# Kernel tuning notes

Hardware: AMD Instinct MI355X
Metric: run time of the kernel (lower is better)

Reference implementation:

```python
import jax, jax.numpy as jnp
import numpy as np

B, T, D_IN, H, OUT = 256, 512, 128, 256, 128


def setup_inputs() -> dict:
    key = jax.random.key(0)
    ks = jax.random.split(key, 10)
    s_in = 1.0 / np.sqrt(H)
    inp = {
        "x": jax.random.normal(ks[0], (B, T, D_IN), dtype=jnp.float32),
        # layer 0 (PyTorch LSTM gate order: i, f, g, o along 4H)
        "W_ih0": jax.random.uniform(ks[1], (4 * H, D_IN), minval=-s_in, maxval=s_in),
        "W_hh0": jax.random.uniform(ks[2], (4 * H, H), minval=-s_in, maxval=s_in),
        "b_ih0": jax.random.uniform(ks[3], (4 * H,), minval=-s_in, maxval=s_in),
        "b_hh0": jax.random.uniform(ks[4], (4 * H,), minval=-s_in, maxval=s_in),
        # layer 1
        "W_ih1": jax.random.uniform(ks[5], (4 * H, H), minval=-s_in, maxval=s_in),
        "W_hh1": jax.random.uniform(ks[6], (4 * H, H), minval=-s_in, maxval=s_in),
        "b_ih1": jax.random.uniform(ks[7], (4 * H,), minval=-s_in, maxval=s_in),
        "b_hh1": jax.random.uniform(ks[8], (4 * H,), minval=-s_in, maxval=s_in),
        # fc head (bias=False)
        "W_fc": jax.random.uniform(ks[9], (OUT, H), minval=-s_in, maxval=s_in),
    }
    return inp


def _lstm_layer(x_seq, W_ih, W_hh, b_ih, b_hh):
    # x_seq: [B, T, D]; precompute input projection once (big GEMM),
    # leave only the small h@W_hh GEMM inside the sequential scan.
    b, t = x_seq.shape[0], x_seq.shape[1]
    h_dim = W_hh.shape[1]
    x_proj = jnp.einsum('btd,gd->btg', x_seq, W_ih) + b_ih + b_hh  # [B,T,4H]

    def step(carry, xt):
        h, c = carry
        gates = xt + h @ W_hh.T  # [B,4H]
        i, f, g, o = jnp.split(gates, 4, axis=-1)
        i = jax.nn.sigmoid(i)
        f = jax.nn.sigmoid(f)
        g = jnp.tanh(g)
        o = jax.nn.sigmoid(o)
        c = f * c + i * g
        h = o * jnp.tanh(c)
        return (h, c), h

    init = (jnp.zeros((b, h_dim), x_seq.dtype), jnp.zeros((b, h_dim), x_seq.dtype))
    _, hs = jax.lax.scan(step, init, jnp.swapaxes(x_proj, 0, 1))  # hs: [T,B,H]
    return jnp.swapaxes(hs, 0, 1)  # [B,T,H]


def reference(x, W_ih0, W_hh0, b_ih0, b_hh0, W_ih1, W_hh1, b_ih1, b_hh1, W_fc):
    h0 = _lstm_layer(x, W_ih0, W_hh0, b_ih0, b_hh0)   # [B,T,H]
    h1 = _lstm_layer(h0, W_ih1, W_hh1, b_ih1, b_hh1)  # [B,T,H]
    last = h1[:, -1, :]                               # [B,H]
    return last @ W_fc.T                              # [B,OUT]
```

## Files before the change

kernel.cpp:

```cpp
#include <hip/hip_runtime.h>
#include <stdint.h>

#define T_   512
#define H_   256
#define OUTD 128

typedef unsigned long long u64;
typedef __attribute__((ext_vector_type(8))) short s8v;
typedef __attribute__((ext_vector_type(4))) float f4v;

__device__ __forceinline__ f4v mfma16x16x32(s8v a, s8v b, f4v c) {
  return __builtin_amdgcn_mfma_f32_16x16x32_bf16(a, b, c, 0, 0, 0);
}

__device__ __forceinline__ void split_bf16(float f, short &hi, short &lo) {
  unsigned u  = __float_as_uint(f);
  unsigned uh = u & 0xffff0000u;
  hi = (short)(uh >> 16);
  float r = f - __uint_as_float(uh);
  unsigned ur = __float_as_uint(r);
  lo = (short)((ur + 0x7fffu + ((ur >> 16) & 1u)) >> 16);
}

__device__ __forceinline__ unsigned pack_hilo(float f) {
  short hi, lo; split_bf16(f, hi, lo);
  return ((unsigned)(unsigned short)hi << 16) | (unsigned)(unsigned short)lo;
}

__device__ __forceinline__ float sig_(float x) { return 1.f / (1.f + __expf(-x)); }
__device__ __forceinline__ float th_(float x)  { float e = __expf(2.f * x); return 1.f - 2.f / (e + 1.f); }

struct SMem {
  short xhi[16][264], xlo[16][264];
  short hhi[16][264], hlo[16][264];
  float gl[4][16][17];
  float bias[64];
};

template <int LAYER>
__device__ __forceinline__ void lstm_body(
    SMem* sm,
    const float* __restrict__ xin,
    const float* __restrict__ Wih, const float* __restrict__ Whh,
    const float* __restrict__ bih, const float* __restrict__ bhh,
    u64* bx_x,
    u64* bx_own,
    unsigned* rflag,
    float* h1l,
    int g, int mem)
{
  constexpr int KX  = (LAYER == 0) ? 128 : 256;
  constexpr int NKX = KX / 32;
  const int tid = threadIdx.x;
  const int w = tid >> 6, lane = tid & 63, n = lane & 15, q = lane >> 4;
  const int bb = tid >> 4, uu = tid & 15;
  const int B0 = g * 16, U0 = mem * 16;

  s8v wxh[NKX], wxl[NKX], whhh[8], whhl[8];
  {
    const int row = w * 256 + U0 + n;
    #pragma unroll
    for (int kf = 0; kf < NKX; ++kf) {
      s8v vh, vl;
      #pragma unroll
      for (int j = 0; j < 8; ++j) { short hi, lo; split_bf16(Wih[row * KX + kf * 32 + q * 8 + j], hi, lo); vh[j] = hi; vl[j] = lo; }
      wxh[kf] = vh; wxl[kf] = vl;
    }
    #pragma unroll
    for (int kf = 0; kf < 8; ++kf) {
      s8v vh, vl;
      #pragma unroll
      for (int j = 0; j < 8; ++j) { short hi, lo; split_bf16(Whh[row * 256 + kf * 32 + q * 8 + j], hi, lo); vh[j] = hi; vl[j] = lo; }
      whhh[kf] = vh; whhl[kf] = vl;
    }
  }
  if (tid < 64) {
    int gate = tid >> 4, u = tid & 15;
    int grow = gate * 256 + U0 + u;
    sm->bias[tid] = bih[grow] + bhh[grow];
  }

  u64* own = bx_own + (size_t)g * 2 * 4096;
  u64* src = (LAYER == 1) ? (bx_x + (size_t)g * 2 * 4096) : nullptr;
  unsigned* rfg    = rflag + g * 256;
  unsigned* rfself = rfg + mem * 16;

  float c = 0.f;

  for (int s = 0; s < T_; ++s) {
    float xv[8];
    if (LAYER == 0) {
      const float* px = xin + ((size_t)(B0 + bb) * T_ + s) * 128 + uu * 8;
      float4 v0 = *(const float4*)px, v1 = *(const float4*)(px + 4);
      xv[0] = v0.x; xv[1] = v0.y; xv[2] = v0.z; xv[3] = v0.w;
      xv[4] = v1.x; xv[5] = v1.y; xv[6] = v1.z; xv[7] = v1.w;
    }

    if (LAYER == 1) {
      const u64* pbx = src + (size_t)(s & 1) * 4096;
      const unsigned xtag = (unsigned)(s + 1);
      u64 xv64[16]; int it = 0;
      for (;;) {
        bool ok = true;
        #pragma unroll
        for (int i = 0; i < 16; ++i)
          xv64[i] = __hip_atomic_load(&pbx[i * 256 + tid], __ATOMIC_RELAXED, __HIP_MEMORY_SCOPE_AGENT);
        #pragma unroll
        for (int i = 0; i < 16; ++i) ok &= ((unsigned)(xv64[i] >> 32) == xtag);
        if (ok) break;
        if (++it >= 50000) break;
        __builtin_amdgcn_s_sleep(1);
      }
      #pragma unroll
      for (int i = 0; i < 16; ++i) {
        unsigned d = (unsigned)xv64[i];
        sm->xhi[i][tid] = (short)(d >> 16);
        sm->xlo[i][tid] = (short)(d & 0xffffu);
      }
    }

    if (s > 0) {
      const u64* pbh = own + (size_t)((s - 1) & 1) * 4096;
      const unsigned htag = (unsigned)s;
      u64 hv64[16]; int it = 0;
      for (;;) {
        bool ok = true;
        #pragma unroll
        for (int i = 0; i < 16; ++i)
          hv64[i] = __hip_atomic_load(&pbh[i * 256 + tid], __ATOMIC_RELAXED, __HIP_MEMORY_SCOPE_AGENT);
        #pragma unroll
        for (int i = 0; i < 16; ++i) ok &= ((unsigned)(hv64[i] >> 32) == htag);
        if (ok) break;
        if (++it >= 50000) break;
        __builtin_amdgcn_s_sleep(1);
      }
      #pragma unroll
      for (int i = 0; i < 16; ++i) {
        unsigned d = (unsigned)hv64[i];
        sm->hhi[i][tid] = (short)(d >> 16);
        sm->hlo[i][tid] = (short)(d & 0xffffu);
      }
    } else {
      #pragma unroll
      for (int i = 0; i < 16; ++i) { sm->hhi[i][tid] = 0; sm->hlo[i][tid] = 0; }
    }

    if (LAYER == 0) {
      s8v vh, vl;
      #pragma unroll
      for (int j = 0; j < 8; ++j) { short hi, lo; split_bf16(xv[j], hi, lo); vh[j] = hi; vl[j] = lo; }
      *(s8v*)&sm->xhi[bb][uu * 8] = vh;
      *(s8v*)&sm->xlo[bb][uu * 8] = vl;
    }
    __syncthreads();

    if (LAYER == 1 && tid == 0)
      __hip_atomic_store(rfself, (unsigned)(s + 1), __ATOMIC_RELAXED, __HIP_MEMORY_SCOPE_AGENT);

    f4v a0 = {0.f, 0.f, 0.f, 0.f}, a1 = a0, a2 = a0;
    #pragma unroll
    for (int kf = 0; kf < NKX; ++kf) {
      s8v ah = *(const s8v*)&sm->xhi[n][kf * 32 + q * 8];
      s8v al = *(const s8v*)&sm->xlo[n][kf * 32 + q * 8];
      a0 = mfma16x16x32(ah, wxh[kf], a0);
      a1 = mfma16x16x32(al, wxh[kf], a1);
      a2 = mfma16x16x32(ah, wxl[kf], a2);
    }
    #pragma unroll
    for (int kf = 0; kf < 8; ++kf) {
      s8v ah = *(const s8v*)&sm->hhi[n][kf * 32 + q * 8];
      s8v al = *(const s8v*)&sm->hlo[n][kf * 32 + q * 8];
      a0 = mfma16x16x32(ah, whhh[kf], a0);
      a1 = mfma16x16x32(al, whhh[kf], a1);
      a2 = mfma16x16x32(ah, whhl[kf], a2);
    }
    f4v D = a0 + (a1 + a2);
    #pragma unroll
    for (int r = 0; r < 4; ++r) sm->gl[w][q * 4 + r][n] = D[r];
    __syncthreads();

    float pi = sm->gl[0][bb][uu] + sm->bias[uu];
    float pf = sm->gl[1][bb][uu] + sm->bias[16 + uu];
    float pg = sm->gl[2][bb][uu] + sm->bias[32 + uu];
    float po = sm->gl[3][bb][uu] + sm->bias[48 + uu];
    float ig = sig_(pi), fg = sig_(pf), gg = th_(pg), og = sig_(po);
    c = fg * c + ig * gg;
    float h = og * th_(c);

    if (LAYER == 0) {
      if (s >= 2 && w == 0) {
        const unsigned tgt = (unsigned)(s - 1); int it = 0;
        for (;;) {
          unsigned v = (lane < 16)
            ? __hip_atomic_load(&rfg[lane * 16], __ATOMIC_RELAXED, __HIP_MEMORY_SCOPE_AGENT)
            : tgt;
          if (__all((int)(v >= tgt))) break;
          if (++it >= 50000) break;
          __builtin_amdgcn_s_sleep(1);
        }
      }
      __syncthreads();
    }

    u64 val = ((u64)(unsigned)(s + 1) << 32) | (u64)pack_hilo(h);
    __hip_atomic_store(&own[(size_t)(s & 1) * 4096 + bb * 256 + U0 + uu], val,
                       __ATOMIC_RELAXED, __HIP_MEMORY_SCOPE_AGENT);

    if (LAYER == 1 && s == T_ - 1)
      h1l[(B0 + bb) * H_ + U0 + uu] = h;
  }
}

__global__ __launch_bounds__(256, 2) void lstm_fused(
    const float* __restrict__ x,
    const float* __restrict__ Wih0, const float* __restrict__ Whh0,
    const float* __restrict__ bih0, const float* __restrict__ bhh0,
    const float* __restrict__ Wih1, const float* __restrict__ Whh1,
    const float* __restrict__ bih1, const float* __restrict__ bhh1,
    u64* bx0, u64* bx1, unsigned* rflag, float* h1l)
{
  __shared__ SMem sm;
  const int bid = blockIdx.x;
  if (bid < 256) {
    lstm_body<0>(&sm, x, Wih0, Whh0, bih0, bhh0, nullptr, bx0, rflag, nullptr,
                 bid >> 4, bid & 15);
  } else {
    const int b = bid - 256;
    lstm_body<1>(&sm, nullptr, Wih1, Whh1, bih1, bhh1, bx0, bx1, rflag, h1l,
                 b >> 4, b & 15);
  }
}

__global__ void fc_kernel(const float* __restrict__ h1l, const float* __restrict__ Wfc,
                          float* __restrict__ out) {
  __shared__ float hs[H_];
  const int b = blockIdx.x, o = threadIdx.x;
  hs[o]       = h1l[b * H_ + o];
  hs[o + 128] = h1l[b * H_ + o + 128];
  __syncthreads();
  float acc = 0.f;
  #pragma unroll 8
  for (int u = 0; u < H_; u += 4) {
    float4 wv = *(const float4*)&Wfc[o * H_ + u];
    acc += wv.x * hs[u] + wv.y * hs[u + 1] + wv.z * hs[u + 2] + wv.w * hs[u + 3];
  }
  out[b * OUTD + o] = acc;
}

extern "C" void kernel_launch(void* const* d_in, const int* in_sizes, int n_in,
                              void* d_out, int out_size, void* d_ws, size_t ws_size,
                              hipStream_t stream) {
  const float* x    = (const float*)d_in[0];
  const float* Wih0 = (const float*)d_in[1];
  const float* Whh0 = (const float*)d_in[2];
  const float* bih0 = (const float*)d_in[3];
  const float* bhh0 = (const float*)d_in[4];
  const float* Wih1 = (const float*)d_in[5];
  const float* Whh1 = (const float*)d_in[6];
  const float* bih1 = (const float*)d_in[7];
  const float* bhh1 = (const float*)d_in[8];
  const float* Wfc  = (const float*)d_in[9];

  u64*      bx0   = (u64*)d_ws;
  u64*      bx1   = bx0 + 131072;
  unsigned* rflag = (unsigned*)(bx1 + 131072);
  float*    h1l   = (float*)(rflag + 4096);

  hipMemsetAsync(rflag, 0, 4096 * sizeof(unsigned), stream);

  lstm_fused<<<512, 256, 0, stream>>>(x, Wih0, Whh0, bih0, bhh0,
                                      Wih1, Whh1, bih1, bhh1,
                                      bx0, bx1, rflag, h1l);
  fc_kernel<<<256, 128, 0, stream>>>(h1l, Wfc, (float*)d_out);
}
```

Measured before the change: 2.726 ms.

## Merge x/h spin-waits with per-slot pending masks and move layer-1 backpressure wait earlier

Combines the separate layer-1 input and recurrent-state polling loops into one loop that tracks a pending bitmask per slot. Each slot is written to shared memory as soon as its tag matches, and only missing slots are reloaded. The layer-0 wait on layer-1 read flags moves from after the gate math to before the MFMA section, which also drops one __syncthreads per step. The aim is shorter cross-block handoff latency per timestep, at the risk of a subtle race, since the flag wait now rests on the earlier barrier ordering.

```diff
diff --git a/kernel.cpp b/kernel.cpp
--- a/kernel.cpp
+++ b/kernel.cpp
@@ -96,53 +96,53 @@
       xv[4] = v1.x; xv[5] = v1.y; xv[6] = v1.z; xv[7] = v1.w;
     }
 
-    if (LAYER == 1) {
-      const u64* pbx = src + (size_t)(s & 1) * 4096;
-      const unsigned xtag = (unsigned)(s + 1);
-      u64 xv64[16]; int it = 0;
-      for (;;) {
-        bool ok = true;
+    if (s == 0) {
+      #pragma unroll
+      for (int i = 0; i < 16; ++i) { sm->hhi[i][tid] = 0; sm->hlo[i][tid] = 0; }
+    }
+
+    {
+      unsigned pendx = (LAYER == 1) ? 0xffffu : 0u;
+      unsigned pendh = (s > 0) ? 0xffffu : 0u;
+      const u64* pbx = (LAYER == 1) ? (src + (size_t)(s & 1) * 4096) : nullptr;
+      const u64* pbh = own + (size_t)((s - 1) & 1) * 4096;
+      const unsigned xtag = (unsigned)(s + 1), htag = (unsigned)s;
+      int it = 0;
+      while (pendx | pendh) {
+        u64 tx[16], th[16];
+        if (LAYER == 1) {
+          #pragma unroll
+          for (int i = 0; i < 16; ++i)
+            if ((pendx >> i) & 1)
+              tx[i] = __hip_atomic_load(&pbx[i * 256 + tid], __ATOMIC_RELAXED, __HIP_MEMORY_SCOPE_AGENT);
+        }
         #pragma unroll
         for (int i = 0; i < 16; ++i)
-          xv64[i] = __hip_atomic_load(&pbx[i * 256 + tid], __ATOMIC_RELAXED, __HIP_MEMORY_SCOPE_AGENT);
-        #pragma unroll
-        for (int i = 0; i < 16; ++i) ok &= ((unsigned)(xv64[i] >> 32) == xtag);
-        if (ok) break;
-        if (++it >= 50000) break;
-        __builtin_amdgcn_s_sleep(1);
-      }
-      #pragma unroll
-      for (int i = 0; i < 16; ++i) {
-        unsigned d = (unsigned)xv64[i];
-        sm->xhi[i][tid] = (short)(d >> 16);
-        sm->xlo[i][tid] = (short)(d & 0xffffu);
-      }
-    }
-
-    if (s > 0) {
-      const u64* pbh = own + (size_t)((s - 1) & 1) * 4096;
-      const unsigned htag = (unsigned)s;
-      u64 hv64[16]; int it = 0;
-      for (;;) {
-        bool ok = true;
+          if ((pendh >> i) & 1)
+            th[i] = __hip_atomic_load(&pbh[i * 256 + tid], __ATOMIC_RELAXED, __HIP_MEMORY_SCOPE_AGENT);
+        if (LAYER == 1) {
+          #pragma unroll
+          for (int i = 0; i < 16; ++i)
+            if (((pendx >> i) & 1) && (unsigned)(tx[i] >> 32) == xtag) {
+              unsigned d = (unsigned)tx[i];
+              sm->xhi[i][tid] = (short)(d >> 16);
+              sm->xlo[i][tid] = (short)(d & 0xffffu);
+              pendx &= ~(1u << i);
+            }
+        }
         #pragma unroll
         for (int i = 0; i < 16; ++i)
-          hv64[i] = __hip_atomic_load(&pbh[i * 256 + tid], __ATOMIC_RELAXED, __HIP_MEMORY_SCOPE_AGENT);
-        #pragma unroll
-        for (int i = 0; i < 16; ++i) ok &= ((unsigned)(hv64[i] >> 32) == htag);
-        if (ok) break;
-        if (++it >= 50000) break;
-        __builtin_amdgcn_s_sleep(1);
+          if (((pendh >> i) & 1) && (unsigned)(th[i] >> 32) == htag) {
+            unsigned d = (unsigned)th[i];
+            sm->hhi[i][tid] = (short)(d >> 16);
+            sm->hlo[i][tid] = (short)(d & 0xffffu);
+            pendh &= ~(1u << i);
+          }
+        if (pendx | pendh) {
+          if (++it >= 50000) break;
+          __builtin_amdgcn_s_sleep(1);
+        }
       }
-      #pragma unroll
-      for (int i = 0; i < 16; ++i) {
-        unsigned d = (unsigned)hv64[i];
-        sm->hhi[i][tid] = (short)(d >> 16);
-        sm->hlo[i][tid] = (short)(d & 0xffffu);
-      }
-    } else {
-      #pragma unroll
-      for (int i = 0; i < 16; ++i) { sm->hhi[i][tid] = 0; sm->hlo[i][tid] = 0; }
     }
 
     if (LAYER == 0) {
@@ -156,6 +156,18 @@
 
     if (LAYER == 1 && tid == 0)
       __hip_atomic_store(rfself, (unsigned)(s + 1), __ATOMIC_RELAXED, __HIP_MEMORY_SCOPE_AGENT);
+
+    if (LAYER == 0 && s >= 2 && w == 0) {
+      const unsigned tgt = (unsigned)(s - 1); int it2 = 0;
+      for (;;) {
+        unsigned v = (lane < 16)
+          ? __hip_atomic_load(&rfg[lane * 16], __ATOMIC_RELAXED, __HIP_MEMORY_SCOPE_AGENT)
+          : tgt;
+        if (__all((int)(v >= tgt))) break;
+        if (++it2 >= 50000) break;
+        __builtin_amdgcn_s_sleep(1);
+      }
+    }
 
     f4v a0 = {0.f, 0.f, 0.f, 0.f}, a1 = a0, a2 = a0;
     #pragma unroll
@@ -186,21 +198,6 @@
     float ig = sig_(pi), fg = sig_(pf), gg = th_(pg), og = sig_(po);
     c = fg * c + ig * gg;
     float h = og * th_(c);
-
-    if (LAYER == 0) {
-      if (s >= 2 && w == 0) {
-        const unsigned tgt = (unsigned)(s - 1); int it = 0;
-        for (;;) {
-          unsigned v = (lane < 16)
-            ? __hip_atomic_load(&rfg[lane * 16], __ATOMIC_RELAXED, __HIP_MEMORY_SCOPE_AGENT)
-            : tgt;
-          if (__all((int)(v >= tgt))) break;
-          if (++it >= 50000) break;
-          __builtin_amdgcn_s_sleep(1);
-        }
-      }
-      __syncthreads();
-    }
 
     u64 val = ((u64)(unsigned)(s + 1) << 32) | (u64)pack_hilo(h);
     __hip_atomic_store(&own[(size_t)(s & 1) * 4096 + bb * 256 + U0 + uu], val,
```

New measurement: 4.300 ms. 57.7% more time.

## Replace per-element tag polling with per-block progress flags for step handoff

Applied to the files above, without the earlier changes.

Adds per-block progress counters that each block publishes after writing its hidden state for a step. Wave 0 polls the peer flags, the upstream-layer flags and the reverse-flow flags in one spin loop, then releases the block with a barrier. The previous layer-0 wait after the gate math is dropped. The intent is to cut the cost of spinning on many tagged 64-bit loads, at the price of an extra barrier and a flag store per step. Stores are relaxed with no release fence, so whether the data is visible before the flag is questionable.

```diff
diff --git a/kernel.cpp b/kernel.cpp
--- a/kernel.cpp
+++ b/kernel.cpp
@@ -46,6 +46,8 @@
     u64* bx_x,
     u64* bx_own,
     unsigned* rflag,
+    unsigned* pf_src,
+    unsigned* pf_own,
     float* h1l,
     int g, int mem)
 {
@@ -84,6 +86,8 @@
   u64* src = (LAYER == 1) ? (bx_x + (size_t)g * 2 * 4096) : nullptr;
   unsigned* rfg    = rflag + g * 256;
   unsigned* rfself = rfg + mem * 16;
+  unsigned* pfs = (LAYER == 1) ? (pf_src + g * 16) : nullptr;
+  unsigned* pfo = pf_own + g * 16;
 
   float c = 0.f;
 
@@ -96,6 +100,26 @@
       xv[4] = v1.x; xv[5] = v1.y; xv[6] = v1.z; xv[7] = v1.w;
     }
 
+    if (w == 0) {
+      int it = 0;
+      for (;;) {
+        bool ok = true;
+        if (lane < 16) {
+          if (s > 0)
+            ok = __hip_atomic_load(&pfo[lane], __ATOMIC_RELAXED, __HIP_MEMORY_SCOPE_AGENT) >= (unsigned)s;
+        } else if (lane < 32) {
+          if (LAYER == 1)
+            ok = __hip_atomic_load(&pfs[lane - 16], __ATOMIC_RELAXED, __HIP_MEMORY_SCOPE_AGENT) >= (unsigned)(s + 1);
+          else if (s >= 2)
+            ok = __hip_atomic_load(&rfg[(lane - 16) * 16], __ATOMIC_RELAXED, __HIP_MEMORY_SCOPE_AGENT) >= (unsigned)(s - 1);
+        }
+        if (__all((int)ok)) break;
+        if (++it >= 200000) break;
+        __builtin_amdgcn_s_sleep(1);
+      }
+    }
+    __syncthreads();
+
     if (LAYER == 1) {
       const u64* pbx = src + (size_t)(s & 1) * 4096;
       const unsigned xtag = (unsigned)(s + 1);
@@ -187,24 +211,13 @@
     c = fg * c + ig * gg;
     float h = og * th_(c);
 
-    if (LAYER == 0) {
-      if (s >= 2 && w == 0) {
-        const unsigned tgt = (unsigned)(s - 1); int it = 0;
-        for (;;) {
-          unsigned v = (lane < 16)
-            ? __hip_atomic_load(&rfg[lane * 16], __ATOMIC_RELAXED, __HIP_MEMORY_SCOPE_AGENT)
-            : tgt;
-          if (__all((int)(v >= tgt))) break;
-          if (++it >= 50000) break;
-          __builtin_amdgcn_s_sleep(1);
-        }
-      }
-      __syncthreads();
-    }
-
     u64 val = ((u64)(unsigned)(s + 1) << 32) | (u64)pack_hilo(h);
     __hip_atomic_store(&own[(size_t)(s & 1) * 4096 + bb * 256 + U0 + uu], val,
                        __ATOMIC_RELAXED, __HIP_MEMORY_SCOPE_AGENT);
+
+    __syncthreads();
+    if (tid == 0)
+      __hip_atomic_store(&pfo[mem], (unsigned)(s + 1), __ATOMIC_RELAXED, __HIP_MEMORY_SCOPE_AGENT);
 
     if (LAYER == 1 && s == T_ - 1)
       h1l[(B0 + bb) * H_ + U0 + uu] = h;
@@ -217,17 +230,18 @@
     const float* __restrict__ bih0, const float* __restrict__ bhh0,
     const float* __restrict__ Wih1, const float* __restrict__ Whh1,
     const float* __restrict__ bih1, const float* __restrict__ bhh1,
-    u64* bx0, u64* bx1, unsigned* rflag, float* h1l)
+    u64* bx0, u64* bx1, unsigned* rflag, unsigned* flag0, unsigned* flag1,
+    float* h1l)
 {
   __shared__ SMem sm;
   const int bid = blockIdx.x;
   if (bid < 256) {
-    lstm_body<0>(&sm, x, Wih0, Whh0, bih0, bhh0, nullptr, bx0, rflag, nullptr,
-                 bid >> 4, bid & 15);
+    lstm_body<0>(&sm, x, Wih0, Whh0, bih0, bhh0, nullptr, bx0, rflag,
+                 nullptr, flag0, nullptr, bid >> 4, bid & 15);
   } else {
     const int b = bid - 256;
-    lstm_body<1>(&sm, nullptr, Wih1, Whh1, bih1, bhh1, bx0, bx1, rflag, h1l,
-                 b >> 4, b & 15);
+    lstm_body<1>(&sm, nullptr, Wih1, Whh1, bih1, bhh1, bx0, bx1, rflag,
+                 flag0, flag1, h1l, b >> 4, b & 15);
   }
 }
 
@@ -264,12 +278,14 @@
   u64*      bx0   = (u64*)d_ws;
   u64*      bx1   = bx0 + 131072;
   unsigned* rflag = (unsigned*)(bx1 + 131072);
-  float*    h1l   = (float*)(rflag + 4096);
-
-  hipMemsetAsync(rflag, 0, 4096 * sizeof(unsigned), stream);
+  unsigned* flag0 = rflag + 4096;
+  unsigned* flag1 = flag0 + 256;
+  float*    h1l   = (float*)(flag1 + 256);
+
+  hipMemsetAsync(rflag, 0, (4096 + 512) * sizeof(unsigned), stream);
 
   lstm_fused<<<512, 256, 0, stream>>>(x, Wih0, Whh0, bih0, bhh0,
                                       Wih1, Whh1, bih1, bhh1,
-                                      bx0, bx1, rflag, h1l);
+                                      bx0, bx1, rflag, flag0, flag1, h1l);
   fc_kernel<<<256, 128, 0, stream>>>(h1l, Wfc, (float*)d_out);
 }
```

After: 3.381 ms. 24.0% more time.

## Deepen layer-0 to layer-1 handoff ring to four slots and prefetch flags

Applied to the files above, without the earlier changes.

Enlarges the layer-0 output ring buffer from two to four slots, so layer 0 may run up to three steps ahead of layer 1 before waiting on the reader flags. The layer-1 input loads and the layer-0 flag read are now issued early in the step and checked later, so their latency overlaps the hidden-state polling. This is meant to cut stalls in the cross-layer producer/consumer pipeline, at the cost of a larger workspace and more live registers.

```diff
diff --git a/kernel.cpp b/kernel.cpp
--- a/kernel.cpp
+++ b/kernel.cpp
@@ -51,6 +51,7 @@
 {
   constexpr int KX  = (LAYER == 0) ? 128 : 256;
   constexpr int NKX = KX / 32;
+  constexpr int OD  = (LAYER == 0) ? 4 : 2;
   const int tid = threadIdx.x;
   const int w = tid >> 6, lane = tid & 63, n = lane & 15, q = lane >> 4;
   const int bb = tid >> 4, uu = tid & 15;
@@ -80,8 +81,8 @@
     sm->bias[tid] = bih[grow] + bhh[grow];
   }
 
-  u64* own = bx_own + (size_t)g * 2 * 4096;
-  u64* src = (LAYER == 1) ? (bx_x + (size_t)g * 2 * 4096) : nullptr;
+  u64* own = bx_own + (size_t)g * OD * 4096;
+  u64* src = (LAYER == 1) ? (bx_x + (size_t)g * 4 * 4096) : nullptr;
   unsigned* rfg    = rflag + g * 256;
   unsigned* rfself = rfg + mem * 16;
 
@@ -96,31 +97,20 @@
       xv[4] = v1.x; xv[5] = v1.y; xv[6] = v1.z; xv[7] = v1.w;
     }
 
+    unsigned rfv = 0xffffffffu;
+    if (LAYER == 0 && s >= 4 && w == 0 && lane < 16)
+      rfv = __hip_atomic_load(&rfg[lane * 16], __ATOMIC_RELAXED, __HIP_MEMORY_SCOPE_AGENT);
+
+    u64 xp[16];
     if (LAYER == 1) {
-      const u64* pbx = src + (size_t)(s & 1) * 4096;
-      const unsigned xtag = (unsigned)(s + 1);
-      u64 xv64[16]; int it = 0;
-      for (;;) {
-        bool ok = true;
-        #pragma unroll
-        for (int i = 0; i < 16; ++i)
-          xv64[i] = __hip_atomic_load(&pbx[i * 256 + tid], __ATOMIC_RELAXED, __HIP_MEMORY_SCOPE_AGENT);
-        #pragma unroll
-        for (int i = 0; i < 16; ++i) ok &= ((unsigned)(xv64[i] >> 32) == xtag);
-        if (ok) break;
-        if (++it >= 50000) break;
-        __builtin_amdgcn_s_sleep(1);
-      }
-      #pragma unroll
-      for (int i = 0; i < 16; ++i) {
-        unsigned d = (unsigned)xv64[i];
-        sm->xhi[i][tid] = (short)(d >> 16);
-        sm->xlo[i][tid] = (short)(d & 0xffffu);
-      }
+      const u64* pbx = src + (size_t)(s & 3) * 4096;
+      #pragma unroll
+      for (int i = 0; i < 16; ++i)
+        xp[i] = __hip_atomic_load(&pbx[i * 256 + tid], __ATOMIC_RELAXED, __HIP_MEMORY_SCOPE_AGENT);
     }
 
     if (s > 0) {
-      const u64* pbh = own + (size_t)((s - 1) & 1) * 4096;
+      const u64* pbh = own + (size_t)((s - 1) & (OD - 1)) * 4096;
       const unsigned htag = (unsigned)s;
       u64 hv64[16]; int it = 0;
       for (;;) {
@@ -145,6 +135,34 @@
       for (int i = 0; i < 16; ++i) { sm->hhi[i][tid] = 0; sm->hlo[i][tid] = 0; }
     }
 
+    if (LAYER == 1) {
+      const u64* pbx = src + (size_t)(s & 3) * 4096;
+      const unsigned xtag = (unsigned)(s + 1);
+      bool ok = true;
+      #pragma unroll
+      for (int i = 0; i < 16; ++i) ok &= ((unsigned)(xp[i] >> 32) == xtag);
+      if (!ok) {
+        int it = 0;
+        for (;;) {
+          ok = true;
+          #pragma unroll
+          for (int i = 0; i < 16; ++i)
+            xp[i] = __hip_atomic_load(&pbx[i * 256 + tid], __ATOMIC_RELAXED, __HIP_MEMORY_SCOPE_AGENT);
+          #pragma unroll
+          for (int i = 0; i < 16; ++i) ok &= ((unsigned)(xp[i] >> 32) == xtag);
+          if (ok) break;
+          if (++it >= 50000) break;
+          __builtin_amdgcn_s_sleep(1);
+        }
+      }
+      #pragma unroll
+      for (int i = 0; i < 16; ++i) {
+        unsigned d = (unsigned)xp[i];
+        sm->xhi[i][tid] = (short)(d >> 16);
+        sm->xlo[i][tid] = (short)(d & 0xffffu);
+      }
+    }
+
     if (LAYER == 0) {
       s8v vh, vl;
       #pragma unroll
@@ -188,22 +206,26 @@
     float h = og * th_(c);
 
     if (LAYER == 0) {
-      if (s >= 2 && w == 0) {
-        const unsigned tgt = (unsigned)(s - 1); int it = 0;
-        for (;;) {
-          unsigned v = (lane < 16)
-            ? __hip_atomic_load(&rfg[lane * 16], __ATOMIC_RELAXED, __HIP_MEMORY_SCOPE_AGENT)
-            : tgt;
-          if (__all((int)(v >= tgt))) break;
-          if (++it >= 50000) break;
-          __builtin_amdgcn_s_sleep(1);
+      if (s >= 4 && w == 0) {
+        const unsigned tgt = (unsigned)(s - 3);
+        bool ok = (lane < 16) ? (rfv >= tgt) : true;
+        if (!__all((int)ok)) {
+          int it = 0;
+          for (;;) {
+            unsigned v = (lane < 16)
+              ? __hip_atomic_load(&rfg[lane * 16], __ATOMIC_RELAXED, __HIP_MEMORY_SCOPE_AGENT)
+              : tgt;
+            if (__all((int)(v >= tgt))) break;
+            if (++it >= 50000) break;
+            __builtin_amdgcn_s_sleep(1);
+          }
         }
       }
       __syncthreads();
     }
 
     u64 val = ((u64)(unsigned)(s + 1) << 32) | (u64)pack_hilo(h);
-    __hip_atomic_store(&own[(size_t)(s & 1) * 4096 + bb * 256 + U0 + uu], val,
+    __hip_atomic_store(&own[(size_t)(s & (OD - 1)) * 4096 + bb * 256 + U0 + uu], val,
                        __ATOMIC_RELAXED, __HIP_MEMORY_SCOPE_AGENT);
 
     if (LAYER == 1 && s == T_ - 1)
@@ -262,7 +284,7 @@
   const float* Wfc  = (const float*)d_in[9];
 
   u64*      bx0   = (u64*)d_ws;
-  u64*      bx1   = bx0 + 131072;
+  u64*      bx1   = bx0 + 262144;
   unsigned* rflag = (unsigned*)(bx1 + 131072);
   float*    h1l   = (float*)(rflag + 4096);
 
```

Measured after the change: 2.785 ms. +2.1%, slower.
